# Kernel tuning notes

Measured on AMD Instinct MI355X. Metric: run time of the kernel, lower is better.

The kernel has to match this reference:

```python
import jax, jax.numpy as jnp
import numpy as np

ANCHORS = np.array([[116, 90], [156, 198], [373, 326],
                    [30, 61], [62, 45], [59, 119],
                    [10, 13], [16, 30], [33, 23]], dtype=np.float32)
IMG = 416.0
NUM_CLASSES = 80
IGNORE_THR = 0.5
SUB_BY_S = {13: 0, 26: 3, 52: 6}  # subtract_index per feature size


def setup_inputs() -> dict:
    key = jax.random.key(0)
    k1, k2, k3, k4 = jax.random.split(key, 4)
    B, N, S = 32, 32, 52
    output = jax.random.normal(k1, (B, 255, S, S), dtype=jnp.float32)
    xy = jax.random.uniform(k2, (B, N, 2), minval=10.0, maxval=406.0)
    wh = jax.random.uniform(k3, (B, N, 2), minval=10.0, maxval=120.0)
    cls = jax.random.randint(k4, (B, N, 1), 0, NUM_CLASSES).astype(jnp.float32)
    targets = jnp.concatenate([xy, wh, cls], axis=-1)  # [B, N, 5] pixel units
    return {"output": output, "targets": targets}


def _bce(p, t):
    eps = 1e-7
    p = jnp.clip(p, eps, 1.0 - eps)
    return -t * jnp.log(p) - (1.0 - t) * jnp.log(1.0 - p)


def _yolo_loss(output, targets):
    B, _, S, _ = output.shape
    C = NUM_CLASSES
    stride = IMG / S
    scaled = jnp.asarray(ANCHORS) / stride          # [9,2] anchors in feature units
    sub = SUB_BY_S[S]

    pred = output.reshape(B, 3, 5 + C, S, S).transpose(0, 1, 3, 4, 2)  # [B,3,S,S,85]
    x = jax.nn.sigmoid(pred[..., 0])
    y = jax.nn.sigmoid(pred[..., 1])
    w = pred[..., 2]
    h = pred[..., 3]
    conf = jax.nn.sigmoid(pred[..., 4])
    pred_cls = jax.nn.sigmoid(pred[..., 5:])

    # ---- get_target (vectorized anchor matching + scatter into grid) ----
    gx = targets[..., 0] / stride                    # [B,N]
    gy = targets[..., 1] / stride
    gw = targets[..., 2] / stride
    gh = targets[..., 3] / stride
    gi = jnp.floor(gx).astype(jnp.int32)
    gj = jnp.floor(gy).astype(jnp.int32)

    aw, ah = scaled[:, 0], scaled[:, 1]              # [9]
    # IoU of (0,0,gw,gh) vs (0,0,aw,ah): centered boxes -> overlap = min(w)*min(h)
    inter = jnp.minimum(gw[..., None], aw) * jnp.minimum(gh[..., None], ah)
    union = gw[..., None] * gh[..., None] + aw * ah - inter
    best = jnp.argmax(inter / union, axis=-1)        # [B,N] best of 9 anchors
    valid = (best >= sub) & (best < sub + 3)
    k = best - sub

    size = B * 3 * S * S
    bidx = jnp.arange(B, dtype=jnp.int32)[:, None]
    flat = (((bidx * 3 + k) * S + gj) * S + gi)      # [i, best_n-sub, gj, gi]
    flat = jnp.where(valid, flat, size)              # sentinel -> dropped
    fr = flat.ravel()

    def scat(vals):
        return jnp.zeros(size, jnp.float32).at[fr].set(
            vals.ravel(), mode='drop').reshape(B, 3, S, S)

    mask = scat(jnp.ones_like(gx))
    noobj = jnp.ones(size, jnp.float32).at[fr].set(0.0, mode='drop').reshape(B, 3, S, S)
    tx = scat(gx - gi.astype(jnp.float32))
    ty = scat(gy - gj.astype(jnp.float32))
    tw = scat(jnp.log(gw / scaled[best, 0]))
    th = scat(jnp.log(gh / scaled[best, 1]))
    bls_x = scat(targets[..., 2] / IMG)
    bls_y = scat(targets[..., 3] / IMG)

    cls_id = targets[..., 4].astype(jnp.int32)
    flat_c = jnp.where(valid, flat * C + cls_id, size * C)
    tcls = jnp.zeros(size * C, jnp.float32).at[flat_c.ravel()].set(
        1.0, mode='drop').reshape(B, 3, S, S, C)

    # ---- get_ignore (pred boxes vs gt boxes, IoU threshold mask) ----
    grid = jnp.arange(S, dtype=jnp.float32)
    la = scaled[sub:sub + 3]                         # [3,2] layer anchors
    px = x + grid[None, None, None, :]
    py = y + grid[None, None, :, None]
    pw = jnp.exp(w) * la[:, 0][None, :, None, None]
    ph = jnp.exp(h) * la[:, 1][None, :, None, None]
    pb = jax.lax.stop_gradient(
        jnp.stack([px, py, pw, ph], axis=-1).reshape(B, -1, 4))  # [B,M,4]

    ax1, ax2 = gx - gw / 2, gx + gw / 2              # [B,N]
    ay1, ay2 = gy - gh / 2, gy + gh / 2
    bx1 = pb[..., 0] - pb[..., 2] / 2                # [B,M]
    bx2 = pb[..., 0] + pb[..., 2] / 2
    by1 = pb[..., 1] - pb[..., 3] / 2
    by2 = pb[..., 1] + pb[..., 3] / 2
    iw = jnp.clip(jnp.minimum(ax2[:, :, None], bx2[:, None, :]) -
                  jnp.maximum(ax1[:, :, None], bx1[:, None, :]), 0.0)
    ih = jnp.clip(jnp.minimum(ay2[:, :, None], by2[:, None, :]) -
                  jnp.maximum(ay1[:, :, None], by1[:, None, :]), 0.0)
    inter2 = iw * ih                                 # [B,N,M]
    area_a = (gw * gh)[:, :, None]
    area_b = (pb[..., 2] * pb[..., 3])[:, None, :]
    iou = inter2 / (area_a + area_b - inter2)
    iou_max = jnp.max(iou, axis=1).reshape(B, 3, S, S)
    noobj = jnp.where(iou_max > IGNORE_THR, 0.0, noobj)

    # ---- losses ----
    box_loss_scale = 2.0 - bls_x * bls_y
    loss_x = jnp.sum(_bce(x, tx) / B * box_loss_scale * mask)
    loss_y = jnp.sum(_bce(y, ty) / B * box_loss_scale * mask)
    loss_w = jnp.sum((w - tw) ** 2 / B * 0.5 * box_loss_scale * mask)
    loss_h = jnp.sum((h - th) ** 2 / B * 0.5 * box_loss_scale * mask)
    bce_conf = _bce(conf, mask)
    loss_conf = jnp.sum(bce_conf * mask / B) + jnp.sum(bce_conf * noobj / B)
    loss_cls = jnp.sum(_bce(pred_cls, tcls) * mask[..., None] / B)

    loss = loss_x + loss_y + loss_w + loss_h + loss_conf + loss_cls
    num_pos = jnp.maximum(jnp.sum(mask), 1.0)
    return loss, num_pos


def reference(output, targets):
    return _yolo_loss(output, targets)
```

## Files before the change

kernel.cpp:

```cpp
#include <hip/hip_runtime.h>
#include <hip/hip_bf16.h>

#define B_    32
#define N_    32
#define S_    52
#define C_    80
#define PLANE (S_*S_)
#define CPB   (3*PLANE)
#define TOT   (B_*CPB)
#define NBLK  (TOT/256)
#define IGNORE_THR 0.5f

__device__ __constant__ float d_aw[9] = {14.5f, 19.5f, 46.625f, 3.75f, 7.75f, 7.375f, 1.25f, 2.0f,  4.125f};
__device__ __constant__ float d_ah[9] = {11.25f,24.75f,40.75f,  7.625f,5.625f,14.875f,1.625f,3.75f, 2.875f};

__global__ void kzero(float* res) {
    if (threadIdx.x < 2) res[threadIdx.x] = 0.0f;
}
__global__ void kfix(float* res) {
    res[1] = fmaxf(res[1], 1.0f);
}

__launch_bounds__(256)
__global__ void kmain(const float* __restrict__ pred,
                      const float* __restrict__ tgts,
                      float2* __restrict__ part,
                      float* __restrict__ res,
                      int use_part) {
    __shared__ float s_ax1[64], s_ay1[64], s_ax2[64], s_ay2[64], s_area[64];
    __shared__ int   s_meta[64];
    __shared__ float s_red[8];

    const int g   = blockIdx.x*256 + (int)threadIdx.x;
    const int b   = g / CPB;
    const int r   = g - b*CPB;
    const int a   = r / PLANE;
    const int lin = r - a*PLANE;
    const int i   = lin / S_;
    const int j   = lin - i*S_;

    const float* base = pred + ((size_t)(b*255 + a*85))*PLANE + lin;
    const float z0 = base[0];
    const float z1 = base[1*PLANE];
    const float z2 = base[2*PLANE];
    const float z3 = base[3*PLANE];
    const float z4 = base[4*PLANE];

    const int bFirst = (blockIdx.x*256) / CPB;
    const int bLast  = (blockIdx.x*256 + 255) / CPB;
    const int nb     = bLast - bFirst + 1;
    if ((int)threadIdx.x < nb * 32) {
        const int n  = threadIdx.x & 31;
        const int bb = bFirst + ((int)threadIdx.x >> 5);
        const float* tp = tgts + (size_t)(bb*N_ + n)*5;
        const float t0 = tp[0], t1 = tp[1], t2 = tp[2], t3 = tp[3], t4 = tp[4];
        const float gx = t0*0.125f, gy = t1*0.125f, gw = t2*0.125f, gh = t3*0.125f;
        int best = 0; float bestr = -1.0f;
        #pragma unroll
        for (int cc = 0; cc < 9; cc++) {
            const float inter = fminf(gw, d_aw[cc]) * fminf(gh, d_ah[cc]);
            const float uni   = gw*gh + d_aw[cc]*d_ah[cc] - inter;
            const float rr    = inter / uni;
            if (rr > bestr) { bestr = rr; best = cc; }
        }
        const int valid = (best >= 6 && best < 9) ? 1 : 0;
        const int gi = (int)floorf(gx);
        const int gj = (int)floorf(gy);
        s_ax1[threadIdx.x]  = gx - gw*0.5f;
        s_ay1[threadIdx.x]  = gy - gh*0.5f;
        s_ax2[threadIdx.x]  = gx + gw*0.5f;
        s_ay2[threadIdx.x]  = gy + gh*0.5f;
        s_area[threadIdx.x] = gw * gh;
        s_meta[threadIdx.x] = valid | (best << 1) | (gi << 5) | (gj << 11) | (((int)t4) << 17);
    }
    __syncthreads();

    const float la_w = (a == 0) ? 1.25f  : ((a == 1) ? 2.0f  : 4.125f);
    const float la_h = (a == 0) ? 1.625f : ((a == 1) ? 3.75f : 2.875f);
    const float sx = 1.0f/(1.0f + __expf(-z0));
    const float sy = 1.0f/(1.0f + __expf(-z1));
    const float px = sx + (float)j;
    const float py = sy + (float)i;
    const float pw = __expf(z2) * la_w;
    const float ph = __expf(z3) * la_h;
    const float bx1 = px - pw*0.5f, bx2 = px + pw*0.5f;
    const float by1 = py - ph*0.5f, by2 = py + ph*0.5f;
    const float areab = pw * ph;

    bool ignore = false;
    int  lastm  = -1;
    unsigned long long cm_lo = 0ull;
    unsigned int       cm_hi = 0u;
    const int sbase = (b - bFirst) * 32;
    #pragma unroll 4
    for (int n = 0; n < N_; n++) {
        const float ax1 = s_ax1[sbase+n], ay1 = s_ay1[sbase+n];
        const float ax2 = s_ax2[sbase+n], ay2 = s_ay2[sbase+n];
        const float ar  = s_area[sbase+n];
        const int meta  = s_meta[sbase+n];
        const float iw = fmaxf(fminf(ax2, bx2) - fmaxf(ax1, bx1), 0.0f);
        const float ih = fmaxf(fminf(ay2, by2) - fmaxf(ay1, by1), 0.0f);
        const float inter = iw * ih;
        ignore = ignore || (3.0f*inter > ar + areab);
        const int mvalid = meta & 1;
        const int mbest  = (meta >> 1) & 15;
        const int mgi    = (meta >> 5) & 63;
        const int mgj    = (meta >> 11) & 63;
        if (mvalid && ((mbest - 6) == a) && (mgj == i) && (mgi == j)) {
            lastm = n;
            const int mcls = (meta >> 17) & 127;
            if (mcls < 64) cm_lo |= 1ull << mcls;
            else           cm_hi |= 1u << (mcls - 64);
        }
    }

    const float eps  = 1e-7f;
    const float invB = 1.0f / (float)B_;
    float loss = 0.0f, npos = 0.0f;

    float conf = 1.0f/(1.0f + __expf(-z4));
    conf = fminf(fmaxf(conf, eps), 1.0f - eps);
    if (lastm < 0) {
        if (!ignore) loss = -__logf(1.0f - conf) * invB;
    } else {
        npos = 1.0f;
        loss = -__logf(conf) * invB;
        const float* tp = tgts + (size_t)(b*N_ + lastm)*5;
        const float t0 = tp[0], t1 = tp[1], t2 = tp[2], t3 = tp[3];
        const float gx = t0*0.125f, gy = t1*0.125f, gw = t2*0.125f, gh = t3*0.125f;
        const float ttx = gx - floorf(gx);
        const float tty = gy - floorf(gy);
        const int   meta  = s_meta[sbase + lastm];
        const int   mbest = (meta >> 1) & 15;
        const float ttw = __logf(gw / d_aw[mbest]);
        const float tth = __logf(gh / d_ah[mbest]);
        const float tbls = 2.0f - (t2/416.0f)*(t3/416.0f);

        float x = fminf(fmaxf(sx, eps), 1.0f - eps);
        float y = fminf(fmaxf(sy, eps), 1.0f - eps);
        const float bx = -ttx*__logf(x) - (1.0f - ttx)*__logf(1.0f - x);
        const float by = -tty*__logf(y) - (1.0f - tty)*__logf(1.0f - y);
        const float dw = z2 - ttw;
        const float dh = z3 - tth;
        loss += (bx + by + 0.5f*dw*dw + 0.5f*dh*dh) * tbls * invB;

        const float* cbase = pred + ((size_t)(b*255 + a*85 + 5))*PLANE + lin;
        #pragma unroll 4
        for (int cc = 0; cc < C_; cc++) {
            const float z = cbase[(size_t)cc * PLANE];
            float p = 1.0f/(1.0f + __expf(-z));
            p = fminf(fmaxf(p, eps), 1.0f - eps);
            const bool t = (cc < 64) ? ((cm_lo >> cc) & 1ull)
                                     : ((cm_hi >> (cc - 64)) & 1u);
            loss += (t ? -__logf(p) : -__logf(1.0f - p)) * invB;
        }
    }

    #pragma unroll
    for (int off = 32; off > 0; off >>= 1) {
        loss += __shfl_down(loss, off, 64);
        npos += __shfl_down(npos, off, 64);
    }
    if ((threadIdx.x & 63) == 0) {
        s_red[(threadIdx.x >> 6)*2 + 0] = loss;
        s_red[(threadIdx.x >> 6)*2 + 1] = npos;
    }
    __syncthreads();
    if (threadIdx.x == 0) {
        float L = 0.0f, P = 0.0f;
        #pragma unroll
        for (int w = 0; w < 4; w++) { L += s_red[2*w]; P += s_red[2*w+1]; }
        if (use_part) part[blockIdx.x] = make_float2(L, P);
        else { atomicAdd(res + 0, L); atomicAdd(res + 1, P); }
    }
}

__launch_bounds__(256)
__global__ void kfinal(const float2* __restrict__ part, float* __restrict__ res) {
    __shared__ float s_red[8];
    float L = 0.0f, P = 0.0f;
    for (int k = threadIdx.x; k < NBLK; k += 256) {
        const float2 v = part[k];
        L += v.x; P += v.y;
    }
    #pragma unroll
    for (int off = 32; off > 0; off >>= 1) {
        L += __shfl_down(L, off, 64);
        P += __shfl_down(P, off, 64);
    }
    if ((threadIdx.x & 63) == 0) {
        s_red[(threadIdx.x >> 6)*2 + 0] = L;
        s_red[(threadIdx.x >> 6)*2 + 1] = P;
    }
    __syncthreads();
    if (threadIdx.x == 0) {
        float tl = 0.0f, tp = 0.0f;
        #pragma unroll
        for (int w = 0; w < 4; w++) { tl += s_red[2*w]; tp += s_red[2*w+1]; }
        res[0] = tl;
        res[1] = fmaxf(tp, 1.0f);
    }
}

extern "C" void kernel_launch(void* const* d_in, const int* in_sizes, int n_in,
                              void* d_out, int out_size, void* d_ws, size_t ws_size,
                              hipStream_t stream) {
    const float* pred = (const float*)d_in[0];
    const float* tgts = (const float*)d_in[1];
    float* res = (float*)d_out;

    if (ws_size >= (size_t)NBLK * sizeof(float2)) {
        float2* part = (float2*)d_ws;
        kmain<<<NBLK, 256, 0, stream>>>(pred, tgts, part, res, 1);
        kfinal<<<1, 256, 0, stream>>>(part, res);
    } else {
        kzero<<<1, 64, 0, stream>>>(res);
        kmain<<<NBLK, 256, 0, stream>>>(pred, tgts, nullptr, res, 0);
        kfix<<<1, 1, 0, stream>>>(res);
    }
}
```

Measured before the change: 140.4 us.

## Distribute class-loss loop across wavefront lanes and precompute target regressions in LDS

```diff
diff --git a/kernel.cpp b/kernel.cpp
--- a/kernel.cpp
+++ b/kernel.cpp
@@ -9,7 +9,6 @@
 #define CPB   (3*PLANE)
 #define TOT   (B_*CPB)
 #define NBLK  (TOT/256)
-#define IGNORE_THR 0.5f
 
 __device__ __constant__ float d_aw[9] = {14.5f, 19.5f, 46.625f, 3.75f, 7.75f, 7.375f, 1.25f, 2.0f,  4.125f};
 __device__ __constant__ float d_ah[9] = {11.25f,24.75f,40.75f,  7.625f,5.625f,14.875f,1.625f,3.75f, 2.875f};
@@ -20,6 +19,9 @@
 __global__ void kfix(float* res) {
     res[1] = fmaxf(res[1], 1.0f);
 }
+
+__device__ __forceinline__ float sigm(float z)  { return 1.0f / (1.0f + __expf(-z)); }
+__device__ __forceinline__ float clampp(float p){ return fminf(fmaxf(p, 1e-7f), 1.0f - 1e-7f); }
 
 __launch_bounds__(256)
 __global__ void kmain(const float* __restrict__ pred,
@@ -27,9 +29,11 @@
                       float2* __restrict__ part,
                       float* __restrict__ res,
                       int use_part) {
-    __shared__ float s_ax1[64], s_ay1[64], s_ax2[64], s_ay2[64], s_area[64];
-    __shared__ int   s_meta[64];
-    __shared__ float s_red[8];
+    __shared__ float4 s_box[64];
+    __shared__ float2 s_am[64];
+    __shared__ float4 s_reg[64];
+    __shared__ float  s_bls[64];
+    __shared__ float  s_red[8];
 
     const int g   = blockIdx.x*256 + (int)threadIdx.x;
     const int b   = g / CPB;
@@ -39,12 +43,12 @@
     const int i   = lin / S_;
     const int j   = lin - i*S_;
 
-    const float* base = pred + ((size_t)(b*255 + a*85))*PLANE + lin;
-    const float z0 = base[0];
-    const float z1 = base[1*PLANE];
-    const float z2 = base[2*PLANE];
-    const float z3 = base[3*PLANE];
-    const float z4 = base[4*PLANE];
+    const int off5 = (b*255 + a*85)*PLANE + lin;
+    const float z0 = pred[off5];
+    const float z1 = pred[off5 + 1*PLANE];
+    const float z2 = pred[off5 + 2*PLANE];
+    const float z3 = pred[off5 + 3*PLANE];
+    const float z4 = pred[off5 + 4*PLANE];
 
     const int bFirst = (blockIdx.x*256) / CPB;
     const int bLast  = (blockIdx.x*256 + 255) / CPB;
@@ -66,19 +70,20 @@
         const int valid = (best >= 6 && best < 9) ? 1 : 0;
         const int gi = (int)floorf(gx);
         const int gj = (int)floorf(gy);
-        s_ax1[threadIdx.x]  = gx - gw*0.5f;
-        s_ay1[threadIdx.x]  = gy - gh*0.5f;
-        s_ax2[threadIdx.x]  = gx + gw*0.5f;
-        s_ay2[threadIdx.x]  = gy + gh*0.5f;
-        s_area[threadIdx.x] = gw * gh;
-        s_meta[threadIdx.x] = valid | (best << 1) | (gi << 5) | (gj << 11) | (((int)t4) << 17);
+        const int key = valid ? (((best - 6) << 12) | (gj << 6) | gi) : 16383;
+        const int meta = key | (((int)t4) << 14);
+        s_box[threadIdx.x] = make_float4(gx - gw*0.5f, gy - gh*0.5f, gx + gw*0.5f, gy + gh*0.5f);
+        s_am[threadIdx.x]  = make_float2(gw * gh, __int_as_float(meta));
+        s_reg[threadIdx.x] = make_float4(gx - (float)gi, gy - (float)gj,
+                                         __logf(gw / d_aw[best]), __logf(gh / d_ah[best]));
+        s_bls[threadIdx.x] = 2.0f - (t2*(1.0f/416.0f))*(t3*(1.0f/416.0f));
     }
     __syncthreads();
 
     const float la_w = (a == 0) ? 1.25f  : ((a == 1) ? 2.0f  : 4.125f);
     const float la_h = (a == 0) ? 1.625f : ((a == 1) ? 3.75f : 2.875f);
-    const float sx = 1.0f/(1.0f + __expf(-z0));
-    const float sy = 1.0f/(1.0f + __expf(-z1));
+    const float sx = sigm(z0);
+    const float sy = sigm(z1);
     const float px = sx + (float)j;
     const float py = sy + (float)i;
     const float pw = __expf(z2) * la_w;
@@ -92,68 +97,67 @@
     unsigned long long cm_lo = 0ull;
     unsigned int       cm_hi = 0u;
     const int sbase = (b - bFirst) * 32;
-    #pragma unroll 4
+    const int mykey = (a << 12) | (i << 6) | j;
+    #pragma unroll 8
     for (int n = 0; n < N_; n++) {
-        const float ax1 = s_ax1[sbase+n], ay1 = s_ay1[sbase+n];
-        const float ax2 = s_ax2[sbase+n], ay2 = s_ay2[sbase+n];
-        const float ar  = s_area[sbase+n];
-        const int meta  = s_meta[sbase+n];
-        const float iw = fmaxf(fminf(ax2, bx2) - fmaxf(ax1, bx1), 0.0f);
-        const float ih = fmaxf(fminf(ay2, by2) - fmaxf(ay1, by1), 0.0f);
+        const float4 tb = s_box[sbase+n];
+        const float2 am = s_am[sbase+n];
+        const int  meta = __float_as_int(am.y);
+        const float iw = fmaxf(fminf(tb.z, bx2) - fmaxf(tb.x, bx1), 0.0f);
+        const float ih = fmaxf(fminf(tb.w, by2) - fmaxf(tb.y, by1), 0.0f);
         const float inter = iw * ih;
-        ignore = ignore || (3.0f*inter > ar + areab);
-        const int mvalid = meta & 1;
-        const int mbest  = (meta >> 1) & 15;
-        const int mgi    = (meta >> 5) & 63;
-        const int mgj    = (meta >> 11) & 63;
-        if (mvalid && ((mbest - 6) == a) && (mgj == i) && (mgi == j)) {
+        ignore = ignore || (3.0f*inter > am.x + areab);
+        if ((meta & 16383) == mykey) {
             lastm = n;
-            const int mcls = (meta >> 17) & 127;
+            const int mcls = meta >> 14;
             if (mcls < 64) cm_lo |= 1ull << mcls;
             else           cm_hi |= 1u << (mcls - 64);
         }
     }
 
-    const float eps  = 1e-7f;
     const float invB = 1.0f / (float)B_;
     float loss = 0.0f, npos = 0.0f;
 
-    float conf = 1.0f/(1.0f + __expf(-z4));
-    conf = fminf(fmaxf(conf, eps), 1.0f - eps);
+    const float conf = clampp(sigm(z4));
     if (lastm < 0) {
         if (!ignore) loss = -__logf(1.0f - conf) * invB;
     } else {
         npos = 1.0f;
-        loss = -__logf(conf) * invB;
-        const float* tp = tgts + (size_t)(b*N_ + lastm)*5;
-        const float t0 = tp[0], t1 = tp[1], t2 = tp[2], t3 = tp[3];
-        const float gx = t0*0.125f, gy = t1*0.125f, gw = t2*0.125f, gh = t3*0.125f;
-        const float ttx = gx - floorf(gx);
-        const float tty = gy - floorf(gy);
-        const int   meta  = s_meta[sbase + lastm];
-        const int   mbest = (meta >> 1) & 15;
-        const float ttw = __logf(gw / d_aw[mbest]);
-        const float tth = __logf(gh / d_ah[mbest]);
-        const float tbls = 2.0f - (t2/416.0f)*(t3/416.0f);
-
-        float x = fminf(fmaxf(sx, eps), 1.0f - eps);
-        float y = fminf(fmaxf(sy, eps), 1.0f - eps);
-        const float bx = -ttx*__logf(x) - (1.0f - ttx)*__logf(1.0f - x);
-        const float by = -tty*__logf(y) - (1.0f - tty)*__logf(1.0f - y);
-        const float dw = z2 - ttw;
-        const float dh = z3 - tth;
-        loss += (bx + by + 0.5f*dw*dw + 0.5f*dh*dh) * tbls * invB;
-
-        const float* cbase = pred + ((size_t)(b*255 + a*85 + 5))*PLANE + lin;
-        #pragma unroll 4
-        for (int cc = 0; cc < C_; cc++) {
-            const float z = cbase[(size_t)cc * PLANE];
-            float p = 1.0f/(1.0f + __expf(-z));
-            p = fminf(fmaxf(p, eps), 1.0f - eps);
-            const bool t = (cc < 64) ? ((cm_lo >> cc) & 1ull)
-                                     : ((cm_hi >> (cc - 64)) & 1u);
-            loss += (t ? -__logf(p) : -__logf(1.0f - p)) * invB;
+        const float4 rg  = s_reg[sbase + lastm];
+        const float  bls = s_bls[sbase + lastm];
+        const float x = clampp(sx);
+        const float y = clampp(sy);
+        const float bx = -rg.x*__logf(x) - (1.0f - rg.x)*__logf(1.0f - x);
+        const float by = -rg.y*__logf(y) - (1.0f - rg.y)*__logf(1.0f - y);
+        const float dw = z2 - rg.z;
+        const float dh = z3 - rg.w;
+        loss = (-__logf(conf) + (bx + by + 0.5f*dw*dw + 0.5f*dh*dh) * bls) * invB;
+    }
+
+    {
+        unsigned long long pm = __ballot(lastm >= 0);
+        const int lane = (int)(threadIdx.x & 63);
+        const int myoff = off5 + 5*PLANE;
+        float clsacc = 0.0f;
+        while (pm) {
+            const int src = __ffsll((unsigned long long)pm) - 1;
+            pm &= pm - 1;
+            const int soff          = __shfl(myoff, src, 64);
+            const unsigned int slo0 = (unsigned int)__shfl((int)(cm_lo & 0xffffffffull), src, 64);
+            const unsigned int slo1 = (unsigned int)__shfl((int)(cm_lo >> 32), src, 64);
+            const unsigned int shi  = (unsigned int)__shfl((int)cm_hi, src, 64);
+            const float za = pred[soff + lane*PLANE];
+            const float pa = clampp(sigm(za));
+            const bool  ta = (lane < 32) ? ((slo0 >> lane) & 1u) : ((slo1 >> (lane - 32)) & 1u);
+            clsacc += ta ? -__logf(pa) : -__logf(1.0f - pa);
+            if (lane < 16) {
+                const float zb = pred[soff + (64 + lane)*PLANE];
+                const float pb = clampp(sigm(zb));
+                const bool  tb = (shi >> lane) & 1u;
+                clsacc += tb ? -__logf(pb) : -__logf(1.0f - pb);
+            }
         }
+        loss += clsacc * invB;
     }
 
     #pragma unroll
```

Measured after the change: 117.9 us. 1.19x faster.
